# Performance work log

Measured on AMD Instinct MI355X. Metric: run time of the kernel, lower is better.

The kernel has to match this reference:

```python
import jax, jax.numpy as jnp
import numpy as np
from jax import lax


def _box_conv3d(x, win):
    k = jnp.ones((1, 1, win, win, win), x.dtype) / float(win ** 3)
    pad = win // 2
    return lax.conv_general_dilated(
        x, k,
        window_strides=(1, 1, 1),
        padding=[(pad, pad)] * 3,
        dimension_numbers=('NCDHW', 'OIDHW', 'NCDHW'),
    )


def setup_inputs() -> dict:
    key = jax.random.key(0)
    k1, k2 = jax.random.split(key)
    shape = (1, 1, 160, 192, 224)
    pred = jax.random.uniform(k1, shape, dtype=jnp.float32)
    target = jax.random.uniform(k2, shape, dtype=jnp.float32)
    return {'pred': pred, 'target': target, 'window_size': 9}


def reference(pred, target, window_size):
    Ii = target
    Ji = pred
    win = window_size
    mu1 = _box_conv3d(Ii, win)
    mu2 = _box_conv3d(Ji, win)
    mu1_sq = mu1 * mu1
    mu2_sq = mu2 * mu2
    mu1_mu2 = mu1 * mu2
    sigma1_sq = _box_conv3d(Ii * Ii, win) - mu1_sq
    sigma2_sq = _box_conv3d(Ji * Ji, win) - mu2_sq
    sigma12 = _box_conv3d(Ii * Ji, win) - mu1_mu2
    eps = jnp.finfo(sigma12.dtype).eps
    cc = sigma12 * sigma12 / jnp.maximum(sigma1_sq * sigma2_sq, eps)
    return -jnp.mean(cc)
```

## Files before the change

### kernel.cpp

```cpp
#include <hip/hip_runtime.h>
#include <hip/hip_fp16.h>

#define D_  160
#define H_  192
#define W_  224
#define HW_ (H_ * W_)
#define HW2_ (HW_ / 2)
#define N_  (D_ * H_ * W_)
#define INV729 (1.0f / 729.0f)
#define HSEG 16
#define NSEG (H_ / HSEG)
#define NROW (HSEG + 9)
#define UPD  (NSEG * 2)


__global__ void k_init(double* acc) { *acc = 0.0; }

__device__ __forceinline__ unsigned pack2(float a, float b) {
    const __half2 h = __floats2half2_rn(a, b);
    return *(const unsigned*)&h;
}

__global__ __launch_bounds__(256) void k_passWH(const float* __restrict__ pred,
                                                const float* __restrict__ targ,
                                                uint4* __restrict__ outA,
                                                unsigned* __restrict__ outB) {
    __shared__ __attribute__((aligned(16))) float lds[4][2][2][128];
    const int wid  = threadIdx.x >> 6;
    const int lane = threadIdx.x & 63;
    const int unit = blockIdx.x * 4 + wid;
    const int d    = unit / UPD;
    const int rem  = unit % UPD;
    const int half = rem & 1;
    const int h0   = (rem >> 1) * HSEG;
    const long dbase = (long)d * HW_;
    const int wbase = half * 112;

    const bool isld = (lane < 60);
    const int  arr  = (lane >= 30) ? 1 : 0;
    const int  j    = arr ? lane - 30 : lane;
    const int  ws   = wbase - 4 + 4 * j;
    const bool ldok = isld && (ws >= 0) && (ws + 3 < W_);
    const float* gsrc = (arr ? pred : targ) + dbase + ws;

    float2 q[5][9];
    #pragma unroll
    for (int c = 0; c < 5; ++c)
        #pragma unroll
        for (int k = 0; k < 9; ++k) q[c][k] = make_float2(0.f, 0.f);
    float S0[5] = {0,0,0,0,0}, S1[5] = {0,0,0,0,0};

    auto fetch = [&](int p) -> float4 {
        float4 f = make_float4(0.f, 0.f, 0.f, 0.f);
        const int hh = h0 - 5 + p;
        if (ldok && hh >= 0 && hh < H_)
            f = *(const float4*)(gsrc + (long)hh * W_);
        return f;
    };

    float4 pfE = fetch(0);
    float4 pfO = fetch(1);
    if (isld) *(float4*)&lds[wid][0][arr][4 * j] = pfE;
    pfE = fetch(2);

    #pragma unroll
    for (int p = 0; p < NROW; ++p) {
        const int cur = p & 1;
        if (isld) *(float4*)&lds[wid][cur ^ 1][arr][4 * j] = (cur ? pfE : pfO);
        if (cur) pfE = fetch(p + 3);
        else     pfO = fetch(p + 3);

        if (lane < 56) {
            float a[10], b[10];
            #pragma unroll
            for (int m = 0; m < 5; ++m) {
                const float2 va = *(const float2*)&lds[wid][cur][0][2 * lane + 2 * m];
                const float2 vb = *(const float2*)&lds[wid][cur][1][2 * lane + 2 * m];
                a[2*m] = va.x; a[2*m+1] = va.y;
                b[2*m] = vb.x; b[2*m+1] = vb.y;
            }
            float sI = 0.f, sJ = 0.f, sII = 0.f, sJJ = 0.f, sIJ = 0.f;
            #pragma unroll
            for (int kk = 0; kk < 9; ++kk) {
                sI  += a[kk];          sJ  += b[kk];
                sII += a[kk] * a[kk];  sJJ += b[kk] * b[kk];
                sIJ += a[kk] * b[kk];
            }
            float w0[5], w1[5];
            w0[0] = sI;  w1[0] = sI  + a[9] - a[0];
            w0[1] = sJ;  w1[1] = sJ  + b[9] - b[0];
            w0[2] = sII; w1[2] = sII + a[9]*a[9] - a[0]*a[0];
            w0[3] = sJJ; w1[3] = sJJ + b[9]*b[9] - b[0]*b[0];
            w0[4] = sIJ; w1[4] = sIJ + a[9]*b[9] - a[0]*b[0];

            const int ph = p % 9;
            #pragma unroll
            for (int c = 0; c < 5; ++c) {
                S0[c] += w0[c] - q[c][ph].x;
                S1[c] += w1[c] - q[c][ph].y;
                q[c][ph].x = w0[c];
                q[c][ph].y = w1[c];
            }
            if (p >= 9) {
                const long rb = dbase + (long)(h0 + p - 9) * W_;
                uint4 oA;
                oA.x = pack2(S0[0], S0[1]); oA.y = pack2(S0[2], S0[3]);
                oA.z = pack2(S1[0], S1[1]); oA.w = pack2(S1[2], S1[3]);
                outA[rb / 2 + half * 56 + lane] = oA;
                outB[rb / 2 + half * 56 + lane] = pack2(S0[4], S1[4]);
            }
        }
    }
}

__global__ __launch_bounds__(256) void k_passD(const uint4* __restrict__ bufA,
                                               const unsigned* __restrict__ bufB,
                                               double* __restrict__ acc) {
    const int DSEG = D_ / 8;
    const int p2 = blockIdx.x * blockDim.x + threadIdx.x;
    const int d0 = blockIdx.y * DSEG;

    float2 q[5][9], S[5];
    #pragma unroll
    for (int c = 0; c < 5; ++c) S[c] = make_float2(0.f, 0.f);

    #pragma unroll
    for (int k = 0; k < 9; ++k) {
        const int dd = d0 - 5 + k;
        uint4 va = make_uint4(0u, 0u, 0u, 0u);
        unsigned vb = 0u;
        if (dd >= 0) {
            va = bufA[(long)dd * HW2_ + p2];
            vb = bufB[(long)dd * HW2_ + p2];
        }
        const float2 a01 = __half22float2(*(const __half2*)&va.x);
        const float2 a23 = __half22float2(*(const __half2*)&va.y);
        const float2 b01 = __half22float2(*(const __half2*)&va.z);
        const float2 b23 = __half22float2(*(const __half2*)&va.w);
        const float2 c44 = __half22float2(*(const __half2*)&vb);
        q[0][k] = make_float2(a01.x, b01.x); S[0].x += a01.x; S[0].y += b01.x;
        q[1][k] = make_float2(a01.y, b01.y); S[1].x += a01.y; S[1].y += b01.y;
        q[2][k] = make_float2(a23.x, b23.x); S[2].x += a23.x; S[2].y += b23.x;
        q[3][k] = make_float2(a23.y, b23.y); S[3].x += a23.y; S[3].y += b23.y;
        q[4][k] = make_float2(c44.x, c44.y); S[4].x += c44.x; S[4].y += c44.y;
    }

    float myacc = 0.f;
    #pragma unroll
    for (int j = 0; j < DSEG; ++j) {
        const int dd = d0 + 4 + j;
        uint4 va = make_uint4(0u, 0u, 0u, 0u);
        unsigned vb = 0u;
        if (dd < D_) {
            va = bufA[(long)dd * HW2_ + p2];
            vb = bufB[(long)dd * HW2_ + p2];
        }
        const float2 a01 = __half22float2(*(const __half2*)&va.x);
        const float2 a23 = __half22float2(*(const __half2*)&va.y);
        const float2 b01 = __half22float2(*(const __half2*)&va.z);
        const float2 b23 = __half22float2(*(const __half2*)&va.w);
        const float2 c44 = __half22float2(*(const __half2*)&vb);
        const float2 nv[5] = {
            make_float2(a01.x, b01.x), make_float2(a01.y, b01.y),
            make_float2(a23.x, b23.x), make_float2(a23.y, b23.y),
            make_float2(c44.x, c44.y)
        };
        const int ph = j % 9;
        #pragma unroll
        for (int c = 0; c < 5; ++c) {
            S[c].x += nv[c].x - q[c][ph].x;
            S[c].y += nv[c].y - q[c][ph].y;
            q[c][ph] = nv[c];
        }
        #pragma unroll
        for (int e = 0; e < 2; ++e) {
            const float mu1 = (e ? S[0].y : S[0].x) * INV729;
            const float mu2 = (e ? S[1].y : S[1].x) * INV729;
            const float s1  = (e ? S[2].y : S[2].x) * INV729 - mu1 * mu1;
            const float s2  = (e ? S[3].y : S[3].x) * INV729 - mu2 * mu2;
            const float s12 = (e ? S[4].y : S[4].x) * INV729 - mu1 * mu2;
            const float den = fmaxf(s1 * s2, 1.1920929e-7f);
            myacc += (s12 * s12) / den;
        }
    }

    __shared__ float red[256];
    red[threadIdx.x] = myacc;
    __syncthreads();
    #pragma unroll
    for (int s = 128; s > 0; s >>= 1) {
        if (threadIdx.x < s) red[threadIdx.x] += red[threadIdx.x + s];
        __syncthreads();
    }
    if (threadIdx.x == 0) atomicAdd(acc, (double)red[0]);
}

__global__ void k_fin(const double* __restrict__ acc, float* __restrict__ out) {
    out[0] = (float)(-(*acc) / (double)N_);
}

extern "C" void kernel_launch(void* const* d_in, const int* in_sizes, int n_in,
                              void* d_out, int out_size, void* d_ws, size_t ws_size,
                              hipStream_t stream) {
    const float* pred = (const float*)d_in[0];
    const float* targ = (const float*)d_in[1];

    uint4*    bufA = (uint4*)d_ws;
    unsigned* bufB = (unsigned*)((char*)d_ws + (size_t)(N_ / 2) * 16);
    double*   acc  = (double*)((char*)d_ws + (size_t)(N_ / 2) * 16 + (size_t)(N_ / 2) * 4);
    float*    out  = (float*)d_out;

    k_init<<<1, 1, 0, stream>>>(acc);
    k_passWH<<<D_ * UPD / 4, 256, 0, stream>>>(pred, targ, bufA, bufB);
    dim3 g3(HW2_ / 256, 8);
    k_passD<<<g3, 256, 0, stream>>>(bufA, bufB, acc);
    k_fin<<<1, 1, 0, stream>>>(acc, out);
}
```

Baseline: 61.33 us.

## Fold accumulator init into first pass, deepen row prefetch, shrink H segment

Removes the separate init kernel launch by zeroing the accumulator from the first block of the W/H pass. Row fetches become unconditional loads with clamped addresses and a select to zero, so the loads are not predicated. The prefetch depth grows from two rows in flight to four. The H segment shrinks from 16 to 12 rows, which gives more units and parallelism but more halo rows reloaded per segment.

New measurement: 56.49 us. 1.09x faster.

```diff
diff --git a/kernel.cpp b/kernel.cpp
--- a/kernel.cpp
+++ b/kernel.cpp
@@ -8,14 +8,12 @@
 #define HW2_ (HW_ / 2)
 #define N_  (D_ * H_ * W_)
 #define INV729 (1.0f / 729.0f)
-#define HSEG 16
+#define HSEG 12
 #define NSEG (H_ / HSEG)
 #define NROW (HSEG + 9)
 #define UPD  (NSEG * 2)
 
 
-__global__ void k_init(double* acc) { *acc = 0.0; }
-
 __device__ __forceinline__ unsigned pack2(float a, float b) {
     const __half2 h = __floats2half2_rn(a, b);
     return *(const unsigned*)&h;
@@ -24,8 +22,11 @@
 __global__ __launch_bounds__(256) void k_passWH(const float* __restrict__ pred,
                                                 const float* __restrict__ targ,
                                                 uint4* __restrict__ outA,
-                                                unsigned* __restrict__ outB) {
+                                                unsigned* __restrict__ outB,
+                                                double* __restrict__ acc) {
     __shared__ __attribute__((aligned(16))) float lds[4][2][2][128];
+    if (blockIdx.x == 0 && threadIdx.x == 0) *acc = 0.0;
+
     const int wid  = threadIdx.x >> 6;
     const int lane = threadIdx.x & 63;
     const int unit = blockIdx.x * 4 + wid;
@@ -38,10 +39,11 @@
 
     const bool isld = (lane < 60);
     const int  arr  = (lane >= 30) ? 1 : 0;
-    const int  j    = arr ? lane - 30 : lane;
-    const int  ws   = wbase - 4 + 4 * j;
-    const bool ldok = isld && (ws >= 0) && (ws + 3 < W_);
-    const float* gsrc = (arr ? pred : targ) + dbase + ws;
+    const int  jj   = arr ? lane - 30 : lane;
+    const int  ws   = wbase - 4 + 4 * jj;
+    const bool geom = isld && (ws >= 0) && (ws + 3 < W_);
+    const int  wsc  = ws < 0 ? 0 : (ws > W_ - 4 ? W_ - 4 : ws);
+    const float* gsrc = (arr ? pred : targ) + dbase + wsc;
 
     float2 q[5][9];
     #pragma unroll
@@ -51,31 +53,29 @@
     float S0[5] = {0,0,0,0,0}, S1[5] = {0,0,0,0,0};
 
     auto fetch = [&](int p) -> float4 {
-        float4 f = make_float4(0.f, 0.f, 0.f, 0.f);
         const int hh = h0 - 5 + p;
-        if (ldok && hh >= 0 && hh < H_)
-            f = *(const float4*)(gsrc + (long)hh * W_);
+        const int hc = hh < 0 ? 0 : (hh >= H_ ? H_ - 1 : hh);
+        float4 f = *(const float4*)(gsrc + (long)hc * W_);
+        if (!(geom && hh >= 0 && hh < H_)) f = make_float4(0.f, 0.f, 0.f, 0.f);
         return f;
     };
 
-    float4 pfE = fetch(0);
-    float4 pfO = fetch(1);
-    if (isld) *(float4*)&lds[wid][0][arr][4 * j] = pfE;
-    pfE = fetch(2);
+    float4 pf[4];
+    pf[0] = fetch(0); pf[1] = fetch(1); pf[2] = fetch(2); pf[3] = fetch(3);
+    if (isld) *(float4*)&lds[wid][0][arr][4 * jj] = pf[0];
+    pf[0] = fetch(4);
 
     #pragma unroll
     for (int p = 0; p < NROW; ++p) {
-        const int cur = p & 1;
-        if (isld) *(float4*)&lds[wid][cur ^ 1][arr][4 * j] = (cur ? pfE : pfO);
-        if (cur) pfE = fetch(p + 3);
-        else     pfO = fetch(p + 3);
+        if (isld) *(float4*)&lds[wid][(p + 1) & 1][arr][4 * jj] = pf[(p + 1) & 3];
+        pf[(p + 1) & 3] = fetch(p + 5);
 
         if (lane < 56) {
             float a[10], b[10];
             #pragma unroll
             for (int m = 0; m < 5; ++m) {
-                const float2 va = *(const float2*)&lds[wid][cur][0][2 * lane + 2 * m];
-                const float2 vb = *(const float2*)&lds[wid][cur][1][2 * lane + 2 * m];
+                const float2 va = *(const float2*)&lds[wid][p & 1][0][2 * lane + 2 * m];
+                const float2 vb = *(const float2*)&lds[wid][p & 1][1][2 * lane + 2 * m];
                 a[2*m] = va.x; a[2*m+1] = va.y;
                 b[2*m] = vb.x; b[2*m+1] = vb.y;
             }
@@ -210,8 +210,7 @@
     double*   acc  = (double*)((char*)d_ws + (size_t)(N_ / 2) * 16 + (size_t)(N_ / 2) * 4);
     float*    out  = (float*)d_out;
 
-    k_init<<<1, 1, 0, stream>>>(acc);
-    k_passWH<<<D_ * UPD / 4, 256, 0, stream>>>(pred, targ, bufA, bufB);
+    k_passWH<<<D_ * UPD / 4, 256, 0, stream>>>(pred, targ, bufA, bufB, acc);
     dim3 g3(HW2_ / 256, 8);
     k_passD<<<g3, 256, 0, stream>>>(bufA, bufB, acc);
     k_fin<<<1, 1, 0, stream>>>(acc, out);
```
